# Kernel optimization log

Hardware: AMD Instinct MI355X
Metric: run time of the kernel (lower is better)

## Reference

```python
import jax, jax.numpy as jnp
import numpy as np


def setup_inputs() -> dict:
    key = jax.random.key(0)
    k1, k2, k3 = jax.random.split(key, 3)
    B, N, L, K, H = 8, 256, 32, 3, 64
    X = jax.random.normal(k1, (B, N, N, L), dtype=jnp.float32)
    G = jax.random.uniform(k2, (K, N, N), dtype=jnp.float32)
    W = jax.random.normal(k3, (K * K * L, H), dtype=jnp.float32) * (2.0 / (K * K * L + H)) ** 0.5
    b = jnp.zeros((H,), dtype=jnp.float32)
    return {"X": X, "G": G, "W": W, "b": b}


def reference(X, G, W, b):
    # X: [b, n, c, l], G: [K, N, N] diffusion supports (n == c == N)
    # Stage 1: diffuse along origin-node axis for all K supports at once.
    m1 = jnp.einsum('bncl,knm->kbmcl', X, G)            # [K, b, m, c, l]
    # Stage 2: diffuse along destination-node axis; lay out so flattening
    # (k, j, l) reproduces torch.cat order (o outer, d inner, feature last).
    m2 = jnp.einsum('kbmcl,jcd->bmdkjl', m1, G)         # [b, m, d, K, K, l]
    B, M, D = m2.shape[0], m2.shape[1], m2.shape[2]
    feat = m2.reshape(B, M, D, -1)                      # [b, m, d, K^2 * l]
    H = jnp.einsum('bmdk,kh->bmdh', feat, W) + b        # [b, m, d, hidden]
    return jax.nn.relu(H)
```

## Files before the change

kernel.cpp:

```cpp
#include <hip/hip_runtime.h>
#include <hip/hip_bf16.h>

#define NB 8
#define NN 256
#define NL 32
#define NQ 8192
#define NH 64
#define SL ((size_t)NQ * NN)

typedef __attribute__((ext_vector_type(8))) short short8v;
typedef __attribute__((ext_vector_type(4))) float float4v;
typedef __attribute__((ext_vector_type(16))) float float16v;

static __device__ __forceinline__ ushort f2bf(float f) {
  __hip_bfloat16 h = __float2bfloat16(f);
  return *reinterpret_cast<const ushort*>(&h);
}
static __device__ __forceinline__ uint packbf(float a, float b) {
  return (uint)f2bf(a) | ((uint)f2bf(b) << 16);
}
static __device__ __forceinline__ void gld_lds16(const void* g, void* l) {
  __builtin_amdgcn_global_load_lds(
      (const __attribute__((address_space(1))) unsigned int*)g,
      (__attribute__((address_space(3))) unsigned int*)l, 16, 0, 0);
}

__global__ __launch_bounds__(256) void prep_g(const float* __restrict__ G,
                                              ushort* __restrict__ Gt) {
  __shared__ float t[32][33];
  const int k = blockIdx.z, m0 = blockIdx.x * 32, n0 = blockIdx.y * 32;
  const int tid = threadIdx.x;
  const int c = tid & 31, r8 = tid >> 5;
#pragma unroll
  for (int i = 0; i < 4; ++i) {
    int r = r8 + i * 8;
    t[r][c] = G[((size_t)k * NN + n0 + r) * NN + m0 + c];
  }
  __syncthreads();
#pragma unroll
  for (int i = 0; i < 4; ++i) {
    int rm = r8 + i * 8;
    Gt[((size_t)k * NN + m0 + rm) * NN + n0 + c] = f2bf(t[c][rm]);
  }
}

__global__ __launch_bounds__(256) void prep_wf(const float* __restrict__ W,
                                               ushort* __restrict__ WtF) {
  const int tid = threadIdx.x;
  for (int e = tid; e < 9 * 2 * 2 * 64; e += 256) {
    const int ln = e & 63, hb = (e >> 6) & 1, kp = (e >> 7) & 1, kj = e >> 8;
    const int h = hb * 32 + (ln & 31);
    const int c0 = kj * 32 + kp * 16 + (ln >> 5) * 8;
    ushort v[8];
#pragma unroll
    for (int i = 0; i < 8; ++i) v[i] = f2bf(W[(size_t)(c0 + i) * NH + h]);
    *(ulong2*)(WtF + (size_t)e * 8) = *(ulong2*)v;
  }
}

__global__ __launch_bounds__(256) void prep_x(const float* __restrict__ X,
                                              ushort* __restrict__ Xt) {
  __shared__ float t[32][33];
  const int qt = blockIdx.x;
  const int n0 = blockIdx.y * 32;
  const int b  = blockIdx.z;
  const int tid = threadIdx.x;
  const int c = tid & 31, r8 = tid >> 5;
  const float* Xb = X + (size_t)b * NN * NQ;
  ushort* Xo = Xt + (size_t)b * SL;
  const size_t q0 = (size_t)qt * 32;
#pragma unroll
  for (int i = 0; i < 4; ++i) {
    int r = r8 + i * 8;
    t[r][c] = Xb[(size_t)(n0 + r) * NQ + q0 + c];
  }
  __syncthreads();
#pragma unroll
  for (int i = 0; i < 4; ++i) {
    int l = r8 + i * 8;
    Xo[((size_t)l * NN + qt) * NN + n0 + c] = f2bf(t[c][l]);
  }
}

__global__ __launch_bounds__(256, 2) void gemm2(
    const ushort* __restrict__ Gt, const ushort* __restrict__ Xt,
    ushort* __restrict__ T1) {
  __shared__ ulong2 LDSQ[4096];
  char* base = (char*)LDSQ;

  const int tid = threadIdx.x;
  const int z = blockIdx.z;
  const ushort* Ab = Gt + (size_t)(z % 3) * NN * NN +
                     (size_t)blockIdx.y * 128 * NN;
  const ushort* Bb = Xt + (size_t)(z / 3) * SL +
                     (size_t)blockIdx.x * 128 * NN;
  ushort* Cb = T1 + (size_t)z * SL;

  const int lane = tid & 63;
  const int w  = tid >> 6;
  const int l5 = lane & 31;
  const int h5 = lane >> 5;
  const int wr = (w >> 1) * 64;
  const int wc = (w & 1) * 64;

  auto stage = [&](int q, int qb) {
    const ushort* a = Ab + q * 64;
    const ushort* bsrc = Bb + q * 64;
    char* d1 = base + qb + ((tid & 192) << 4);
    char* d2 = d1 + 16384;
#pragma unroll
    for (int i = 0; i < 4; ++i) {
      const int gl = i * 256 + tid;
      const int R  = gl >> 4;
      const int sd = (gl & 15) ^ (R & 15);
      const int dr = 2 * R + (sd >> 3);
      const int g  = sd & 7;
      gld_lds16(a + (size_t)dr * 256 + g * 8, d1 + (i << 12));
      gld_lds16(bsrc + (size_t)dr * 256 + g * 8, d2 + (i << 12));
    }
  };
  auto ldv = [&](int qb, int toff, int row, int gq) -> short8v {
    const int R = row >> 1;
    const int s = (((row & 1) << 3) + gq) ^ (R & 15);
    return *(const short8v*)(base + qb + toff + (((R << 4) + s) << 4));
  };

  float16v acc[2][2] = {};

  stage(0, 0);

  for (int q = 0; q < 4; ++q) {
    const int qb = (q & 1) << 15;
    __syncthreads();
    if (q + 1 < 4) stage(q + 1, qb ^ 32768);
#pragma unroll
    for (int ks = 0; ks < 4; ++ks) {
      const int gq = 2 * ks + h5;
      short8v a0 = ldv(qb, 0,     wr + l5,      gq);
      short8v a1 = ldv(qb, 0,     wr + 32 + l5, gq);
      short8v b0 = ldv(qb, 16384, wc + l5,      gq);
      short8v b1 = ldv(qb, 16384, wc + 32 + l5, gq);
      acc[0][0] = __builtin_amdgcn_mfma_f32_32x32x16_bf16(a0, b0, acc[0][0], 0, 0, 0);
      acc[0][1] = __builtin_amdgcn_mfma_f32_32x32x16_bf16(a0, b1, acc[0][1], 0, 0, 0);
      acc[1][0] = __builtin_amdgcn_mfma_f32_32x32x16_bf16(a1, b0, acc[1][0], 0, 0, 0);
      acc[1][1] = __builtin_amdgcn_mfma_f32_32x32x16_bf16(a1, b1, acc[1][1], 0, 0, 0);
    }
  }

#pragma unroll
  for (int ms = 0; ms < 2; ++ms) {
#pragma unroll
    for (int ds = 0; ds < 2; ++ds) {
      ushort* cp = Cb +
          (size_t)(blockIdx.y * 128 + wr + ms * 32 + 4 * h5) * NQ +
          blockIdx.x * 128 + wc + ds * 32 + l5;
#pragma unroll
      for (int r = 0; r < 16; ++r) {
        const int row = (r & 3) + 8 * (r >> 2);
        cp[(size_t)row * NQ] = f2bf(acc[ms][ds][r]);
      }
    }
  }
}

__global__ __launch_bounds__(256, 2) void fused_s23(
    const ushort* __restrict__ T1, const ushort* __restrict__ Gt,
    const ushort* __restrict__ WtF, const float* __restrict__ bias,
    float* __restrict__ out) {
  __shared__ ulong2 LDSQ[4096];
  char* base = (char*)LDSQ;

  const int tid = threadIdx.x;
  const int f = blockIdx.x;
  const int lid = (f & 7) * 128 + (f >> 3);
  const int dblk = lid & 1;
  const int mp   = (lid >> 1) & 63;
  const int b    = lid >> 7;

  const int lane = tid & 63;
  const int w  = tid >> 6;
  const int l5 = lane & 31;
  const int h5 = lane >> 5;
  const int wml = (w >> 1) * 64;
  const int wd  = (w & 1) * 64;
  const int d0  = dblk * 128;

  const ushort* t1b  = T1 + ((size_t)b * 3) * SL + (size_t)mp * 128 * 256;
  const ushort* gtb0 = Gt + (size_t)d0 * NN;

  auto stage = [&](int t, int qb) {
    const int kj = t >> 2, q = t & 3;
    const int k = (kj >= 6) ? 2 : (kj >= 3 ? 1 : 0);
    const int j = kj - k * 3;
    const ushort* t1k = t1b + (size_t)k * SL + q * 64;
    const ushort* gtj = gtb0 + (size_t)j * NN * NN + q * 64;
    char* d1 = base + qb + ((tid & 192) << 4);
    char* d2 = d1 + 16384;
#pragma unroll
    for (int i = 0; i < 4; ++i) {
      const int gl = i * 256 + tid;
      const int R  = gl >> 4;
      const int sd = (gl & 15) ^ (R & 15);
      const int dr = 2 * R + (sd >> 3);
      const int g  = sd & 7;
      gld_lds16(t1k + (size_t)dr * 256 + g * 8, d1 + (i << 12));
      gld_lds16(gtj + (size_t)dr * 256 + g * 8, d2 + (i << 12));
    }
  };
  auto ldv = [&](int qb, int toff, int row, int gq) -> short8v {
    const int R = row >> 1;
    const int s = (((row & 1) << 3) + gq) ^ (R & 15);
    return *(const short8v*)(base + qb + toff + (((R << 4) + s) << 4));
  };

  float16v acc3[2][2][2] = {};
  float16v acc2[2][2] = {};

  stage(0, 0);

  for (int t = 0; t < 36; ++t) {
    const int qb = (t & 1) << 15;
    __syncthreads();
    if (t + 1 < 36) stage(t + 1, qb ^ 32768);

#pragma unroll
    for (int ks = 0; ks < 4; ++ks) {
      const int gq = 2 * ks + h5;
      short8v af0 = ldv(qb, 0,     wml + l5,      gq);
      short8v af1 = ldv(qb, 0,     wml + 32 + l5, gq);
      short8v bf0 = ldv(qb, 16384, wd + l5,       gq);
      short8v bf1 = ldv(qb, 16384, wd + 32 + l5,  gq);
      acc2[0][0] = __builtin_amdgcn_mfma_f32_32x32x16_bf16(af0, bf0, acc2[0][0], 0, 0, 0);
      acc2[0][1] = __builtin_amdgcn_mfma_f32_32x32x16_bf16(af0, bf1, acc2[0][1], 0, 0, 0);
      acc2[1][0] = __builtin_amdgcn_mfma_f32_32x32x16_bf16(af1, bf0, acc2[1][0], 0, 0, 0);
      acc2[1][1] = __builtin_amdgcn_mfma_f32_32x32x16_bf16(af1, bf1, acc2[1][1], 0, 0, 0);
    }

    if ((t & 3) == 3) {
      const int kj = t >> 2;
      short8v Af[2][2];
#pragma unroll
      for (int kp = 0; kp < 2; ++kp)
#pragma unroll
        for (int hb = 0; hb < 2; ++hb)
          Af[kp][hb] = *(const short8v*)(WtF +
              ((size_t)(((kj * 2 + kp) * 2 + hb) * 64 + lane)) * 8);

#pragma unroll
      for (int ms = 0; ms < 2; ++ms) {
#pragma unroll
        for (int ds = 0; ds < 2; ++ds) {
          uint P[8];
#pragma unroll
          for (int q = 0; q < 8; ++q)
            P[q] = packbf(acc2[ms][ds][2 * q], acc2[ms][ds][2 * q + 1]);
          short8v Bf[2];
#pragma unroll
          for (int kp = 0; kp < 2; ++kp) {
            uint a0 = P[4 * kp + 0], b0 = P[4 * kp + 2];
            uint a1 = P[4 * kp + 1], b1 = P[4 * kp + 3];
            asm("v_permlane32_swap_b32 %0, %1" : "+v"(a0), "+v"(b0));
            asm("v_permlane32_swap_b32 %0, %1" : "+v"(a1), "+v"(b1));
            uint4 u;
            u.x = a0; u.y = a1; u.z = b0; u.w = b1;
            Bf[kp] = *(short8v*)&u;
          }
#pragma unroll
          for (int hb = 0; hb < 2; ++hb) {
#pragma unroll
            for (int kp = 0; kp < 2; ++kp)
              acc3[ms][ds][hb] = __builtin_amdgcn_mfma_f32_32x32x16_bf16(
                  Af[kp][hb], Bf[kp], acc3[ms][ds][hb], 0, 0, 0);
          }
#pragma unroll
          for (int q = 0; q < 16; ++q) acc2[ms][ds][q] = 0.f;
        }
      }
    }
  }

  float4* EP = (float4*)base;
#pragma unroll
  for (int mlp = 0; mlp < 2; ++mlp) {
    __syncthreads();
    if ((w >> 1) == mlp) {
#pragma unroll
      for (int ms = 0; ms < 2; ++ms) {
#pragma unroll
        for (int ds = 0; ds < 2; ++ds) {
          const int d = wd + ds * 32 + l5;
#pragma unroll
          for (int hb = 0; hb < 2; ++hb) {
#pragma unroll
            for (int s = 0; s < 4; ++s) {
              const int hg = 2 * s + h5 + 8 * hb;
              float4 v;
              v.x = acc3[ms][ds][hb][4 * s + 0];
              v.y = acc3[ms][ds][hb][4 * s + 1];
              v.z = acc3[ms][ds][hb][4 * s + 2];
              v.w = acc3[ms][ds][hb][4 * s + 3];
              EP[(ms * 128 + d) * 16 + (hg ^ (d & 15))] = v;
            }
          }
        }
      }
    }
    __syncthreads();
#pragma unroll
    for (int ii = 0; ii < 16; ++ii) {
      const int fi = tid + ii * 256;
      const int ml = fi >> 11;
      const int d  = (fi >> 4) & 127;
      const int hg = fi & 15;
      float4 v = EP[(ml * 128 + d) * 16 + (hg ^ (d & 15))];
      const float4 bb = *(const float4*)(bias + hg * 4);
      v.x = fmaxf(v.x + bb.x, 0.f);
      v.y = fmaxf(v.y + bb.y, 0.f);
      v.z = fmaxf(v.z + bb.z, 0.f);
      v.w = fmaxf(v.w + bb.w, 0.f);
      const int m = mp * 4 + mlp * 2 + ml;
      float* ob = out + (((size_t)b * NN + m) * NN + d0 + d) * NH;
      *(float4*)(ob + hg * 4) = v;
    }
  }
}

extern "C" void kernel_launch(void* const* d_in, const int* in_sizes, int n_in,
                              void* d_out, int out_size, void* d_ws, size_t ws_size,
                              hipStream_t stream) {
  (void)in_sizes; (void)n_in; (void)out_size; (void)ws_size;
  const float* X    = (const float*)d_in[0];
  const float* G    = (const float*)d_in[1];
  const float* W    = (const float*)d_in[2];
  const float* bias = (const float*)d_in[3];
  float* out = (float*)d_out;

  char* p = (char*)d_ws;
  ushort* Gt  = (ushort*)p;  p += (size_t)3 * NN * NN * 2;
  ushort* WtF = (ushort*)p;  p += (size_t)64 * 1024;
  ushort* Xt  = (ushort*)p;  p += (size_t)NB * SL * 2;
  ushort* T1  = (ushort*)p;

  prep_g<<<dim3(8, 8, 3), 256, 0, stream>>>(G, Gt);
  prep_wf<<<dim3(1), 256, 0, stream>>>(W, WtF);
  prep_x<<<dim3(256, 8, NB), 256, 0, stream>>>(X, Xt);

  gemm2<<<dim3(NQ / 128, NN / 128, 24), 256, 0, stream>>>(Gt, Xt, T1);

  fused_s23<<<dim3(1024), 256, 0, stream>>>(T1, Gt, WtF, bias, out);
}
```

Baseline: 195.1 us.

## Switch stage-2 K loop to triple-buffered 32-wide slices with explicit vmcnt waits

The K-slice per iteration shrinks from 64 to 32 elements, and LDS staging moves from a double buffer (2x32KB) to a three-deep ring (3x16KB). Two slices are prefetched ahead. The __syncthreads is replaced by a partial s_waitcnt vmcnt plus s_barrier, so the next loads can stay in flight while the current slice is consumed. The aim is to hide global-to-LDS latency better and cut LDS footprint, at the cost of twice as many barriers and a swizzle layout that must stay conflict-free.

```diff
diff --git a/kernel.cpp b/kernel.cpp
--- a/kernel.cpp
+++ b/kernel.cpp
@@ -188,92 +188,105 @@
   const ushort* t1b  = T1 + ((size_t)b * 3) * SL + (size_t)mp * 128 * 256;
   const ushort* gtb0 = Gt + (size_t)d0 * NN;
 
-  auto stage = [&](int t, int qb) {
-    const int kj = t >> 2, q = t & 3;
+  auto stage8 = [&](int t2, int sb) {
+    const int kj = t2 >> 3, q8 = t2 & 7;
     const int k = (kj >= 6) ? 2 : (kj >= 3 ? 1 : 0);
     const int j = kj - k * 3;
-    const ushort* t1k = t1b + (size_t)k * SL + q * 64;
-    const ushort* gtj = gtb0 + (size_t)j * NN * NN + q * 64;
-    char* d1 = base + qb + ((tid & 192) << 4);
-    char* d2 = d1 + 16384;
-#pragma unroll
-    for (int i = 0; i < 4; ++i) {
+    const ushort* t1k = t1b + (size_t)k * SL + q8 * 32;
+    const ushort* gtj = gtb0 + (size_t)j * NN * NN + q8 * 32;
+    char* d1 = base + sb + ((tid & 192) << 4);
+    char* d2 = d1 + 8192;
+#pragma unroll
+    for (int i = 0; i < 2; ++i) {
       const int gl = i * 256 + tid;
       const int R  = gl >> 4;
-      const int sd = (gl & 15) ^ (R & 15);
-      const int dr = 2 * R + (sd >> 3);
-      const int g  = sd & 7;
+      const int v  = (gl & 15) ^ (R & 15);
+      const int dr = 4 * R + (v >> 2);
+      const int g  = v & 3;
       gld_lds16(t1k + (size_t)dr * 256 + g * 8, d1 + (i << 12));
       gld_lds16(gtj + (size_t)dr * 256 + g * 8, d2 + (i << 12));
     }
   };
-  auto ldv = [&](int qb, int toff, int row, int gq) -> short8v {
-    const int R = row >> 1;
-    const int s = (((row & 1) << 3) + gq) ^ (R & 15);
-    return *(const short8v*)(base + qb + toff + (((R << 4) + s) << 4));
+  auto ldv8 = [&](int sb, int toff, int row, int gq) -> short8v {
+    const int R = row >> 2;
+    const int s = (((row & 3) << 2) + gq) ^ (R & 15);
+    return *(const short8v*)(base + sb + toff + (((R << 4) + s) << 4));
   };
 
   float16v acc3[2][2][2] = {};
   float16v acc2[2][2] = {};
 
-  stage(0, 0);
-
-  for (int t = 0; t < 36; ++t) {
-    const int qb = (t & 1) << 15;
-    __syncthreads();
-    if (t + 1 < 36) stage(t + 1, qb ^ 32768);
-
-#pragma unroll
-    for (int ks = 0; ks < 4; ++ks) {
-      const int gq = 2 * ks + h5;
-      short8v af0 = ldv(qb, 0,     wml + l5,      gq);
-      short8v af1 = ldv(qb, 0,     wml + 32 + l5, gq);
-      short8v bf0 = ldv(qb, 16384, wd + l5,       gq);
-      short8v bf1 = ldv(qb, 16384, wd + 32 + l5,  gq);
-      acc2[0][0] = __builtin_amdgcn_mfma_f32_32x32x16_bf16(af0, bf0, acc2[0][0], 0, 0, 0);
-      acc2[0][1] = __builtin_amdgcn_mfma_f32_32x32x16_bf16(af0, bf1, acc2[0][1], 0, 0, 0);
-      acc2[1][0] = __builtin_amdgcn_mfma_f32_32x32x16_bf16(af1, bf0, acc2[1][0], 0, 0, 0);
-      acc2[1][1] = __builtin_amdgcn_mfma_f32_32x32x16_bf16(af1, bf1, acc2[1][1], 0, 0, 0);
-    }
-
-    if ((t & 3) == 3) {
-      const int kj = t >> 2;
-      short8v Af[2][2];
-#pragma unroll
-      for (int kp = 0; kp < 2; ++kp)
-#pragma unroll
-        for (int hb = 0; hb < 2; ++hb)
-          Af[kp][hb] = *(const short8v*)(WtF +
-              ((size_t)(((kj * 2 + kp) * 2 + hb) * 64 + lane)) * 8);
-
-#pragma unroll
-      for (int ms = 0; ms < 2; ++ms) {
-#pragma unroll
-        for (int ds = 0; ds < 2; ++ds) {
-          uint P[8];
-#pragma unroll
-          for (int q = 0; q < 8; ++q)
-            P[q] = packbf(acc2[ms][ds][2 * q], acc2[ms][ds][2 * q + 1]);
-          short8v Bf[2];
-#pragma unroll
-          for (int kp = 0; kp < 2; ++kp) {
-            uint a0 = P[4 * kp + 0], b0 = P[4 * kp + 2];
-            uint a1 = P[4 * kp + 1], b1 = P[4 * kp + 3];
-            asm("v_permlane32_swap_b32 %0, %1" : "+v"(a0), "+v"(b0));
-            asm("v_permlane32_swap_b32 %0, %1" : "+v"(a1), "+v"(b1));
-            uint4 u;
-            u.x = a0; u.y = a1; u.z = b0; u.w = b1;
-            Bf[kp] = *(short8v*)&u;
+  stage8(0, 0);
+  stage8(1, 16384);
+
+  for (int tt = 0; tt < 72; tt += 24) {
+#pragma unroll
+    for (int u = 0; u < 24; ++u) {
+      const int t = tt + u;
+      __builtin_amdgcn_sched_barrier(0);
+      if (t == 71) {
+        asm volatile("s_waitcnt vmcnt(0)" ::: "memory");
+      } else {
+        asm volatile("s_waitcnt vmcnt(4)" ::: "memory");
+      }
+      __builtin_amdgcn_s_barrier();
+      __builtin_amdgcn_sched_barrier(0);
+
+      if (t + 2 < 72) stage8(t + 2, ((u + 2) % 3) * 16384);
+
+      const int sb = (u % 3) * 16384;
+#pragma unroll
+      for (int ks = 0; ks < 2; ++ks) {
+        const int gq = 2 * ks + h5;
+        short8v af0 = ldv8(sb, 0,    wml + l5,      gq);
+        short8v af1 = ldv8(sb, 0,    wml + 32 + l5, gq);
+        short8v bf0 = ldv8(sb, 8192, wd + l5,       gq);
+        short8v bf1 = ldv8(sb, 8192, wd + 32 + l5,  gq);
+        acc2[0][0] = __builtin_amdgcn_mfma_f32_32x32x16_bf16(af0, bf0, acc2[0][0], 0, 0, 0);
+        acc2[0][1] = __builtin_amdgcn_mfma_f32_32x32x16_bf16(af0, bf1, acc2[0][1], 0, 0, 0);
+        acc2[1][0] = __builtin_amdgcn_mfma_f32_32x32x16_bf16(af1, bf0, acc2[1][0], 0, 0, 0);
+        acc2[1][1] = __builtin_amdgcn_mfma_f32_32x32x16_bf16(af1, bf1, acc2[1][1], 0, 0, 0);
+      }
+
+      if ((u & 7) == 7) {
+        const int kj = t >> 3;
+        short8v Af[2][2];
+#pragma unroll
+        for (int kp = 0; kp < 2; ++kp)
+#pragma unroll
+          for (int hb = 0; hb < 2; ++hb)
+            Af[kp][hb] = *(const short8v*)(WtF +
+                ((size_t)(((kj * 2 + kp) * 2 + hb) * 64 + lane)) * 8);
+
+#pragma unroll
+        for (int ms = 0; ms < 2; ++ms) {
+#pragma unroll
+          for (int ds = 0; ds < 2; ++ds) {
+            uint P[8];
+#pragma unroll
+            for (int q = 0; q < 8; ++q)
+              P[q] = packbf(acc2[ms][ds][2 * q], acc2[ms][ds][2 * q + 1]);
+            short8v Bf[2];
+#pragma unroll
+            for (int kp = 0; kp < 2; ++kp) {
+              uint a0 = P[4 * kp + 0], b0 = P[4 * kp + 2];
+              uint a1 = P[4 * kp + 1], b1 = P[4 * kp + 3];
+              asm("v_permlane32_swap_b32 %0, %1" : "+v"(a0), "+v"(b0));
+              asm("v_permlane32_swap_b32 %0, %1" : "+v"(a1), "+v"(b1));
+              uint4 uu;
+              uu.x = a0; uu.y = a1; uu.z = b0; uu.w = b1;
+              Bf[kp] = *(short8v*)&uu;
+            }
+#pragma unroll
+            for (int hb = 0; hb < 2; ++hb) {
+#pragma unroll
+              for (int kp = 0; kp < 2; ++kp)
+                acc3[ms][ds][hb] = __builtin_amdgcn_mfma_f32_32x32x16_bf16(
+                    Af[kp][hb], Bf[kp], acc3[ms][ds][hb], 0, 0, 0);
+            }
+#pragma unroll
+            for (int q = 0; q < 16; ++q) acc2[ms][ds][q] = 0.f;
           }
-#pragma unroll
-          for (int hb = 0; hb < 2; ++hb) {
-#pragma unroll
-            for (int kp = 0; kp < 2; ++kp)
-              acc3[ms][ds][hb] = __builtin_amdgcn_mfma_f32_32x32x16_bf16(
-                  Af[kp][hb], Bf[kp], acc3[ms][ds][hb], 0, 0, 0);
-          }
-#pragma unroll
-          for (int q = 0; q < 16; ++q) acc2[ms][ds][q] = 0.f;
         }
       }
     }
```

Result: slower. 200.3 us (+2.7%).
